# Optimization experiments

Hardware: AMD Instinct MI355X
Metric: run time of the kernel (lower is better)

The kernel has to match this reference:

```python
import jax, jax.numpy as jnp
import numpy as np

EPS = 0.1


def setup_inputs() -> dict:
    key = jax.random.key(0)
    x = jax.random.uniform(key, (3, 64, 64), dtype=jnp.float32)
    return {"x": x}


def reference(x):
    # x: [C, H, W]
    C, H, W = x.shape
    N = C * H * W
    a = jax.nn.relu(EPS - x) * 0.5          # shift for x < eps
    b = jax.nn.relu(x - (1.0 - EPS)) * 0.5  # shift for x > 1-eps
    center = x + a - b                       # zonotope center
    err = EPS - a - b                        # per-pixel error coefficient

    flat_err = err.reshape(-1)               # [N], row-major == torch loop order
    mask = flat_err >= 0                     # condition
    # sequential index assignment == prefix sum over the mask (1-based -> row 1..)
    row = jnp.cumsum(mask.astype(jnp.int32))           # [N]
    row = jnp.where(mask, row, N + 1)                  # out-of-range -> dropped
    col = jnp.arange(N, dtype=jnp.int32)

    zono = jnp.zeros((1 + N, N), dtype=x.dtype)
    zono = zono.at[0].set(center.reshape(-1))
    zono = zono.at[row, col].set(flat_err, mode='drop')
    zono = zono.reshape(1 + N, C, H, W)

    # created_terms: [i_error, channel] per created term, -1 padded for skipped elems
    f_idx = col // (H * W)
    terms = jnp.stack([jnp.where(mask, row, -1), jnp.where(mask, f_idx, -1)], axis=-1)
    return zono, terms
```

## Files before the change

kernel.cpp:

```cpp
#include <hip/hip_runtime.h>

#define C_DIM   3
#define H_DIM   64
#define W_DIM   64
#define HW      (H_DIM * W_DIM)
#define N_TOT   (C_DIM * HW)
#define NTHREADS 1024
#define PER     (N_TOT / NTHREADS)
#define EPS_F   0.1f

__global__ __launch_bounds__(NTHREADS) void zono_scatter(
        const float* __restrict__ x,
        float* __restrict__ zono,
        float* __restrict__ terms)
{
    const int tid  = threadIdx.x;
    const int base = tid * PER;

    float cen[PER];
    float ev[PER];
    bool  m[PER];
    int   cnt = 0;

#pragma unroll
    for (int i = 0; i < PER; ++i) {
        float xv = x[base + i];
        float a  = fmaxf(EPS_F - xv, 0.0f) * 0.5f;
        float b  = fmaxf(xv - (1.0f - EPS_F), 0.0f) * 0.5f;
        cen[i]   = xv + a - b;
        float e  = EPS_F - a - b;
        ev[i]    = e;
        m[i]     = (e >= 0.0f);
        cnt     += m[i] ? 1 : 0;
    }

    __shared__ int sh[NTHREADS];
    sh[tid] = cnt;
    __syncthreads();
    for (int off = 1; off < NTHREADS; off <<= 1) {
        int t = (tid >= off) ? sh[tid - off] : 0;
        __syncthreads();
        sh[tid] += t;
        __syncthreads();
    }
    int run = sh[tid] - cnt;

#pragma unroll
    for (int i = 0; i < PER; ++i) {
        const int idx = base + i;
        zono[idx] = cen[i];
        float rowf, fidxf;
        if (m[i]) {
            ++run;
            zono[(size_t)run * N_TOT + idx] = ev[i];
            rowf  = (float)run;
            fidxf = (float)(idx / HW);
        } else {
            rowf  = -1.0f;
            fidxf = -1.0f;
        }
        terms[2 * idx + 0] = rowf;
        terms[2 * idx + 1] = fidxf;
    }
}

extern "C" void kernel_launch(void* const* d_in, const int* in_sizes, int n_in,
                              void* d_out, int out_size, void* d_ws, size_t ws_size,
                              hipStream_t stream) {
    const float* x = (const float*)d_in[0];
    float* out = (float*)d_out;

    const size_t zono_elems = (size_t)(N_TOT + 1) * (size_t)N_TOT;

    hipMemsetAsync(out, 0, zono_elems * sizeof(float), stream);

    zono_scatter<<<1, NTHREADS, 0, stream>>>(x, out, out + zono_elems);
}
```

Baseline: 121.1 us.

## Replace memset plus scatter with a prep kernel and a fused row-fill kernel

```diff
diff --git a/kernel.cpp b/kernel.cpp
--- a/kernel.cpp
+++ b/kernel.cpp
@@ -5,14 +5,22 @@
 #define W_DIM   64
 #define HW      (H_DIM * W_DIM)
 #define N_TOT   (C_DIM * HW)
-#define NTHREADS 1024
-#define PER     (N_TOT / NTHREADS)
+#define PREP_T  1024
+#define PER     (N_TOT / PREP_T)
+#define FILL_T  256
+#define F4_PER_ROW (N_TOT / 4)
+#define F4_PER_THR (F4_PER_ROW / FILL_T)
 #define EPS_F   0.1f
 
-__global__ __launch_bounds__(NTHREADS) void zono_scatter(
+typedef float f4 __attribute__((ext_vector_type(4)));
+
+
+__global__ __launch_bounds__(PREP_T) void zono_prep(
         const float* __restrict__ x,
-        float* __restrict__ zono,
-        float* __restrict__ terms)
+        float* __restrict__ terms,
+        float* __restrict__ center,
+        float* __restrict__ errmap,
+        int*   __restrict__ colmap)
 {
     const int tid  = threadIdx.x;
     const int base = tid * PER;
@@ -32,12 +40,14 @@
         ev[i]    = e;
         m[i]     = (e >= 0.0f);
         cnt     += m[i] ? 1 : 0;
+        center[base + i] = cen[i];
+        colmap[base + i + 1] = -1;
     }
 
-    __shared__ int sh[NTHREADS];
+    __shared__ int sh[PREP_T];
     sh[tid] = cnt;
     __syncthreads();
-    for (int off = 1; off < NTHREADS; off <<= 1) {
+    for (int off = 1; off < PREP_T; off <<= 1) {
         int t = (tid >= off) ? sh[tid - off] : 0;
         __syncthreads();
         sh[tid] += t;
@@ -48,11 +58,11 @@
 #pragma unroll
     for (int i = 0; i < PER; ++i) {
         const int idx = base + i;
-        zono[idx] = cen[i];
         float rowf, fidxf;
         if (m[i]) {
             ++run;
-            zono[(size_t)run * N_TOT + idx] = ev[i];
+            colmap[run] = idx;
+            errmap[run] = ev[i];
             rowf  = (float)run;
             fidxf = (float)(idx / HW);
         } else {
@@ -64,6 +74,38 @@
     }
 }
 
+__global__ __launch_bounds__(FILL_T) void zono_fill(
+        float* __restrict__ zono,
+        const float* __restrict__ center,
+        const float* __restrict__ errmap,
+        const int*   __restrict__ colmap)
+{
+    const int row = blockIdx.x;
+    f4* dst = (f4*)(zono + (size_t)row * N_TOT);
+
+    if (row == 0) {
+        const f4* src = (const f4*)center;
+#pragma unroll
+        for (int k = 0; k < F4_PER_THR; ++k) {
+            int j = threadIdx.x + k * FILL_T;
+            __builtin_nontemporal_store(src[j], &dst[j]);
+        }
+    } else {
+        const int   col = colmap[row];
+        const float ev  = errmap[row];
+        const int patch_j = col >> 2;
+        const int patch_l = col & 3;
+        const f4 z = {0.f, 0.f, 0.f, 0.f};
+#pragma unroll
+        for (int k = 0; k < F4_PER_THR; ++k) {
+            int j = threadIdx.x + k * FILL_T;
+            f4 v = z;
+            v[patch_l] = (j == patch_j) ? ev : v[patch_l];
+            __builtin_nontemporal_store(v, &dst[j]);
+        }
+    }
+}
+
 extern "C" void kernel_launch(void* const* d_in, const int* in_sizes, int n_in,
                               void* d_out, int out_size, void* d_ws, size_t ws_size,
                               hipStream_t stream) {
@@ -71,8 +113,12 @@
     float* out = (float*)d_out;
 
     const size_t zono_elems = (size_t)(N_TOT + 1) * (size_t)N_TOT;
+    float* terms = out + zono_elems;
 
-    hipMemsetAsync(out, 0, zono_elems * sizeof(float), stream);
+    float* center = (float*)d_ws;
+    float* errmap = center + N_TOT;
+    int*   colmap = (int*)(errmap + N_TOT + 1);
 
-    zono_scatter<<<1, NTHREADS, 0, stream>>>(x, out, out + zono_elems);
+    zono_prep<<<1, PREP_T, 0, stream>>>(x, terms, center, errmap, colmap);
+    zono_fill<<<N_TOT + 1, FILL_T, 0, stream>>>(out, center, errmap, colmap);
 }
```

Result: slower. 136.8 us (+12.9%).
